# Performance work log

Measured on AMD Instinct MI355X. Metric: run time of the kernel, lower is better.

## Reference

```python
import jax, jax.numpy as jnp
import numpy as np

NEG = 1e9  # mask value added to already-selected positions (original uses -1e9)


def setup_inputs() -> dict:
    key = jax.random.key(0)
    ks = jax.random.split(key, 12)
    B, N, M = 8, 2048, 256
    s = 0.05  # keep gates/softmax in a sane range
    return dict(
        node_embedding=jax.random.normal(ks[0], (B, N, M), dtype=jnp.float32),
        z_g=jax.random.normal(ks[1], (B, M), dtype=jnp.float32) * s,
        decoder_init=jax.random.normal(ks[2], (M,), dtype=jnp.float32) * s,
        hidden0=jax.random.normal(ks[3], (M,), dtype=jnp.float32) * s,
        w_ih=jax.random.normal(ks[4], (4 * M, M), dtype=jnp.float32) * s,
        w_hh=jax.random.normal(ks[5], (4 * M, M), dtype=jnp.float32) * s,
        b_ih=jax.random.normal(ks[6], (4 * M,), dtype=jnp.float32) * s,
        b_hh=jax.random.normal(ks[7], (4 * M,), dtype=jnp.float32) * s,
        Wq=jax.random.normal(ks[8], (M, M), dtype=jnp.float32) * s,
        bq=jax.random.normal(ks[9], (M,), dtype=jnp.float32) * s,
        Wk=jax.random.normal(ks[10], (M, M), dtype=jnp.float32) * s,
        bk=jax.random.normal(ks[11], (M,), dtype=jnp.float32) * s,
    )


def reference(node_embedding, z_g, decoder_init, hidden0,
              w_ih, w_hh, b_ih, b_hh, Wq, bq, Wk, bk):
    # Returns the per-step masked softmax attention distributions [B, N, N]
    # (row t = distribution over boxes at decode step t; argmax of each row
    #  is the predicted order, and selected indices are masked out).
    N = node_embedding.shape[1]
    # LSTM input is the constant decoder_init every step -> precompute its proj.
    x_proj = decoder_init @ w_ih.T + b_ih  # [4M]

    def decode_one(z_g_b, node_emb_b):
        keys = node_emb_b @ Wk.T + bk  # [N, M] (self.key(node_embedding))

        def step(carry, _):
            h, c, used = carry
            # torch LSTMCell: gates ordered (i, f, g, o)
            gates = x_proj + h @ w_hh.T + b_hh  # [4M]
            i_g, f_g, g_g, o_g = jnp.split(gates, 4)
            i_g = jax.nn.sigmoid(i_g)
            f_g = jax.nn.sigmoid(f_g)
            g_g = jnp.tanh(g_g)
            o_g = jax.nn.sigmoid(o_g)
            c = f_g * c + i_g * g_g
            h = o_g * jnp.tanh(c)
            q = h @ Wq.T + bq                    # [M]
            scores = keys @ q                    # [N]
            scores = jnp.where(used, scores - NEG, scores)  # mask selected
            probs = jax.nn.softmax(scores)       # [N]
            idx = jnp.argmax(probs)              # top-1 pointer selection
            used = used.at[idx].set(True)
            return (h, c, used), probs

        init = (hidden0, z_g_b, jnp.zeros((N,), dtype=bool))
        _, probs = jax.lax.scan(step, init, None, length=N)
        return probs  # [N, N]

    return jax.vmap(decode_one)(z_g, node_embedding)  # [B, N, N]
```

## Files before the change

### kernel.cpp

```cpp
#include <hip/hip_runtime.h>
#include <cstdint>
#include <cstddef>

#define NB 8
#define NN 2048
#define MM 256

typedef unsigned long long u64;

__device__ __forceinline__ unsigned mapf(float f) {
  unsigned u = __float_as_uint(f + 0.f);
  return ((int)u >= 0) ? (u ^ 0x80000000u) : ~u;
}
__device__ __forceinline__ u64 shflx_u64(u64 v, int m) {
  unsigned lo = (unsigned)__shfl_xor((int)(unsigned)v, m);
  unsigned hi = (unsigned)__shfl_xor((int)(v >> 32), m);
  return ((u64)hi << 32) | lo;
}
__device__ __forceinline__ u64 agent_load(const u64* p) {
  return __hip_atomic_load(p, __ATOMIC_RELAXED, __HIP_MEMORY_SCOPE_AGENT);
}

__global__ __launch_bounds__(1024) void lstm_kernel(
    const float* __restrict__ z_g, const float* __restrict__ dec,
    const float* __restrict__ h0, const float* __restrict__ w_ih,
    const float* __restrict__ w_hh, const float* __restrict__ b_ih,
    const float* __restrict__ b_hh, float* __restrict__ Hall,
    u64* __restrict__ Pbuf)
{
  const int b = blockIdx.x;
  const int q = blockIdx.y;
  const int tid = threadIdx.x;
  const int w = tid >> 6;
  const int lane = tid & 63;
  const int rr = lane >> 3;
  const int c8 = lane & 7;
  const int lr = 8 * w + rr;
  const int g = lr >> 5;
  const int m = lr & 31;
  const int grow = g * 256 + 32 * q + m;

  __shared__ __align__(16) float hbuf[256];
  __shared__ __align__(16) float act[128];

  float wreg[32];
  {
    const float* wr = w_hh + (size_t)grow * MM + 32 * c8;
    #pragma unroll
    for (int jj = 0; jj < 8; ++jj) {
      float4 v = *(const float4*)(wr + 4 * ((jj + c8) & 7));
      wreg[4 * jj + 0] = v.x; wreg[4 * jj + 1] = v.y;
      wreg[4 * jj + 2] = v.z; wreg[4 * jj + 3] = v.w;
    }
  }

  float xb;
  {
    const float* wr = w_ih + (size_t)grow * MM + 32 * c8;
    float p = 0.f;
    #pragma unroll
    for (int i = 0; i < 8; ++i) {
      float4 wv = *(const float4*)(wr + 4 * i);
      float4 dv = *(const float4*)(dec + 32 * c8 + 4 * i);
      p += wv.x * dv.x + wv.y * dv.y + wv.z * dv.z + wv.w * dv.w;
    }
    p += __shfl_xor(p, 1); p += __shfl_xor(p, 2); p += __shfl_xor(p, 4);
    xb = p + b_ih[grow] + b_hh[grow];
  }

  float c_my = 0.f;
  if (tid < 32) c_my = z_g[b * MM + 32 * q + tid];
  if (tid < 256) hbuf[tid] = h0[tid];

  u64* Pb = Pbuf + (size_t)b * 512;
  float* Hb = Hall + (size_t)b * NN * MM + 32 * q;

  const bool own0 = ((lane >> 5) + 0) == q;
  const bool own1 = ((lane >> 5) + 2) == q;
  const bool own2 = ((lane >> 5) + 4) == q;
  const bool own3 = ((lane >> 5) + 6) == q;

  for (int tt = 0; tt < NN; ++tt) {
    if (tt > 0 && w == 0) {
      const u64* pa = Pb + ((tt & 1) << 8);
      const unsigned tg = (unsigned)tt;
      u64 a0, a1, a2, a3;
      for (;;) {
        a0 = agent_load(pa + lane);
        a1 = agent_load(pa + 64 + lane);
        a2 = agent_load(pa + 128 + lane);
        a3 = agent_load(pa + 192 + lane);
        const bool ok = (own0 | ((unsigned)(a0 >> 32) == tg))
                      & (own1 | ((unsigned)(a1 >> 32) == tg))
                      & (own2 | ((unsigned)(a2 >> 32) == tg))
                      & (own3 | ((unsigned)(a3 >> 32) == tg));
        if (__all((int)ok)) break;
      }
      if (!own0) hbuf[lane]       = __uint_as_float((unsigned)a0);
      if (!own1) hbuf[64 + lane]  = __uint_as_float((unsigned)a1);
      if (!own2) hbuf[128 + lane] = __uint_as_float((unsigned)a2);
      if (!own3) hbuf[192 + lane] = __uint_as_float((unsigned)a3);
    }
    __syncthreads();

    const float4* h4 = (const float4*)hbuf;
    float a0 = 0.f, a1 = 0.f, a2 = 0.f, a3 = 0.f;
    #pragma unroll
    for (int jj = 0; jj < 8; ++jj) {
      float4 hv = h4[8 * c8 + ((jj + c8) & 7)];
      a0 = fmaf(hv.x, wreg[4 * jj + 0], a0);
      a1 = fmaf(hv.y, wreg[4 * jj + 1], a1);
      a2 = fmaf(hv.z, wreg[4 * jj + 2], a2);
      a3 = fmaf(hv.w, wreg[4 * jj + 3], a3);
    }
    float s = (a0 + a1) + (a2 + a3);
    s += __shfl_xor(s, 1); s += __shfl_xor(s, 2); s += __shfl_xor(s, 4);
    const float gsum = s + xb;

    float a;
    if ((w >> 2) == 2) { const float e = __expf(-2.f * gsum); a = 2.f / (1.f + e) - 1.f; }
    else               { a = 1.f / (1.f + __expf(-gsum)); }
    if (c8 == 0) act[lr] = a;
    __syncthreads();

    if (tid < 32) {
      const float i_g = act[tid], f_g = act[32 + tid];
      const float g_g = act[64 + tid], o_g = act[96 + tid];
      c_my = f_g * c_my + i_g * g_g;
      const float e2 = __expf(-2.f * c_my);
      const float hn = o_g * (2.f / (1.f + e2) - 1.f);
      const u64 pk = ((u64)(unsigned)(tt + 1) << 32) | (u64)__float_as_uint(hn);
      __hip_atomic_store(Pb + (((tt + 1) & 1) << 8) + 32 * q + tid, pk,
                         __ATOMIC_RELAXED, __HIP_MEMORY_SCOPE_AGENT);
      hbuf[32 * q + tid] = hn;
      Hb[(size_t)tt * MM + tid] = hn;
    }
  }
}

__global__ __launch_bounds__(256) void gemm128(
    const float* __restrict__ A, const float* __restrict__ B,
    float* __restrict__ C, const float* __restrict__ bias,
    int K, int Ncol, long sA, long sB, long sC)
{
  __shared__ __align__(16) float As[32][132];
  __shared__ __align__(16) float Bs[32][132];
  const int tid = threadIdx.x;
  const int tx = tid & 15;
  const int ty = tid >> 4;
  const int row0 = blockIdx.y * 128;
  const int col0 = blockIdx.x * 128;
  const float* Ab = A + (size_t)blockIdx.z * (size_t)sA;
  const float* Bb = B + (size_t)blockIdx.z * (size_t)sB;
  float* Cb = C + (size_t)blockIdx.z * (size_t)sC;

  float acc[8][8];
  #pragma unroll
  for (int i = 0; i < 8; ++i)
    #pragma unroll
    for (int jj = 0; jj < 8; ++jj) acc[i][jj] = 0.f;

  for (int k0 = 0; k0 < K; k0 += 32) {
    #pragma unroll
    for (int it = 0; it < 4; ++it) {
      const int idx = tid + it * 256;
      const int r = idx >> 3;
      const int c4 = (idx & 7) << 2;
      float4 va = *(const float4*)(Ab + (size_t)(row0 + r) * K + k0 + c4);
      float4 vb = *(const float4*)(Bb + (size_t)(col0 + r) * K + k0 + c4);
      As[c4 + 0][r] = va.x; As[c4 + 1][r] = va.y;
      As[c4 + 2][r] = va.z; As[c4 + 3][r] = va.w;
      Bs[c4 + 0][r] = vb.x; Bs[c4 + 1][r] = vb.y;
      Bs[c4 + 2][r] = vb.z; Bs[c4 + 3][r] = vb.w;
    }
    __syncthreads();
    #pragma unroll
    for (int kk = 0; kk < 32; ++kk) {
      float4 a0 = *(const float4*)&As[kk][ty * 4];
      float4 a1 = *(const float4*)&As[kk][64 + ty * 4];
      float4 b0 = *(const float4*)&Bs[kk][tx * 4];
      float4 b1 = *(const float4*)&Bs[kk][64 + tx * 4];
      const float av[8] = {a0.x, a0.y, a0.z, a0.w, a1.x, a1.y, a1.z, a1.w};
      const float bv[8] = {b0.x, b0.y, b0.z, b0.w, b1.x, b1.y, b1.z, b1.w};
      #pragma unroll
      for (int i = 0; i < 8; ++i)
        #pragma unroll
        for (int jj = 0; jj < 8; ++jj)
          acc[i][jj] = fmaf(av[i], bv[jj], acc[i][jj]);
    }
    __syncthreads();
  }

  #pragma unroll
  for (int i = 0; i < 8; ++i) {
    const int r = row0 + ((i < 4) ? (ty * 4 + i) : (64 + ty * 4 + i - 4));
    float* cp = Cb + (size_t)r * Ncol + col0;
    float4 o0, o1;
    float* o0p = &o0.x; float* o1p = &o1.x;
    #pragma unroll
    for (int jj = 0; jj < 4; ++jj) {
      float v0 = acc[i][jj], v1 = acc[i][jj + 4];
      if (bias) {
        v0 += bias[col0 + tx * 4 + jj];
        v1 += bias[col0 + 64 + tx * 4 + jj];
      }
      o0p[jj] = v0; o1p[jj] = v1;
    }
    *(float4*)(cp + tx * 4) = o0;
    *(float4*)(cp + 64 + tx * 4) = o1;
  }
}

__global__ __launch_bounds__(512) void select_block(
    const float* __restrict__ S, int* __restrict__ sel)
{
  const int b = blockIdx.x;
  const int tid = threadIdx.x;
  const int w = tid >> 6;
  const int lane = tid & 63;
  const float* Sb = S + (size_t)b * NN * NN + 4 * tid;
  int* selb = sel + b * NN;

  __shared__ u64 partial[2][8];

  for (int i = tid; i < NN; i += 512) selb[i] = 0x7fffffff;
  __syncthreads();

  unsigned mybits = 0;
  const unsigned base = 2047u - 4u * (unsigned)tid;

  auto stepf = [&](float4 v, int t) {
    u64 k0 = (mybits & 1u) ? 0 : (((u64)mapf(v.x) << 32) | (base - 0u));
    u64 k1 = (mybits & 2u) ? 0 : (((u64)mapf(v.y) << 32) | (base - 1u));
    u64 k2 = (mybits & 4u) ? 0 : (((u64)mapf(v.z) << 32) | (base - 2u));
    u64 k3 = (mybits & 8u) ? 0 : (((u64)mapf(v.w) << 32) | (base - 3u));
    u64 k = k0 > k1 ? k0 : k1;
    if (k2 > k) k = k2;
    if (k3 > k) k = k3;
    #pragma unroll
    for (int off = 1; off < 64; off <<= 1) {
      u64 o = shflx_u64(k, off);
      if (o > k) k = o;
    }
    if (lane == 0) partial[t & 1][w] = k;
    __syncthreads();
    u64 pk = partial[t & 1][lane & 7];
    #pragma unroll
    for (int off = 1; off < 8; off <<= 1) {
      u64 o = shflx_u64(pk, off);
      if (o > pk) pk = o;
    }
    const int idx = 2047 - (int)(pk & 0x7ff);
    if ((idx >> 2) == tid) mybits |= 1u << (idx & 3);
    if (tid == 0) selb[idx] = t;
  };

  float4 r0 = *(const float4*)(Sb + (size_t)0 * NN);
  float4 r1 = *(const float4*)(Sb + (size_t)1 * NN);
  float4 r2 = *(const float4*)(Sb + (size_t)2 * NN);
  float4 r3 = *(const float4*)(Sb + (size_t)3 * NN);
  for (int t = 0; t < NN; t += 4) {
    const size_t p4 = (size_t)((t + 4 < NN) ? t + 4 : NN - 1) * NN;
    const size_t p5 = (size_t)((t + 5 < NN) ? t + 5 : NN - 1) * NN;
    const size_t p6 = (size_t)((t + 6 < NN) ? t + 6 : NN - 1) * NN;
    const size_t p7 = (size_t)((t + 7 < NN) ? t + 7 : NN - 1) * NN;
    stepf(r0, t);     r0 = *(const float4*)(Sb + p4);
    stepf(r1, t + 1); r1 = *(const float4*)(Sb + p5);
    stepf(r2, t + 2); r2 = *(const float4*)(Sb + p6);
    stepf(r3, t + 3); r3 = *(const float4*)(Sb + p7);
  }
}

__global__ __launch_bounds__(256) void softmax_kernel(
    float* __restrict__ out, const int* __restrict__ sel)
{
  const int t = blockIdx.x;
  const int b = blockIdx.y;
  const int tid = threadIdx.x;
  float* row = out + ((size_t)b * NN + t) * NN;
  const int* selb = sel + b * NN;
  __shared__ float red[8];

  float v[8];
  int sl[8];
  #pragma unroll
  for (int u = 0; u < 2; ++u) {
    float4 f = *(const float4*)(row + u * 1024 + tid * 4);
    int4 s4 = *(const int4*)(selb + u * 1024 + tid * 4);
    v[u * 4 + 0] = f.x; v[u * 4 + 1] = f.y; v[u * 4 + 2] = f.z; v[u * 4 + 3] = f.w;
    sl[u * 4 + 0] = s4.x; sl[u * 4 + 1] = s4.y; sl[u * 4 + 2] = s4.z; sl[u * 4 + 3] = s4.w;
  }

  float mx = -3.0e38f;
  #pragma unroll
  for (int e = 0; e < 8; ++e)
    if (sl[e] >= t) mx = fmaxf(mx, v[e]);
  #pragma unroll
  for (int off = 1; off < 64; off <<= 1) mx = fmaxf(mx, __shfl_xor(mx, off));
  if ((tid & 63) == 0) red[tid >> 6] = mx;
  __syncthreads();
  mx = fmaxf(fmaxf(red[0], red[1]), fmaxf(red[2], red[3]));

  float e8[8];
  float sum = 0.f;
  #pragma unroll
  for (int e = 0; e < 8; ++e) {
    float ex = (sl[e] >= t) ? __expf(v[e] - mx) : 0.f;
    e8[e] = ex;
    sum += ex;
  }
  #pragma unroll
  for (int off = 1; off < 64; off <<= 1) sum += __shfl_xor(sum, off);
  if ((tid & 63) == 0) red[4 + (tid >> 6)] = sum;
  __syncthreads();
  sum = red[4] + red[5] + red[6] + red[7];
  const float inv = 1.f / sum;

  #pragma unroll
  for (int u = 0; u < 2; ++u) {
    float4 o;
    o.x = e8[u * 4 + 0] * inv; o.y = e8[u * 4 + 1] * inv;
    o.z = e8[u * 4 + 2] * inv; o.w = e8[u * 4 + 3] * inv;
    *(float4*)(row + u * 1024 + tid * 4) = o;
  }
}

extern "C" void kernel_launch(void* const* d_in, const int* in_sizes, int n_in,
                              void* d_out, int out_size, void* d_ws, size_t ws_size,
                              hipStream_t stream)
{
  (void)in_sizes; (void)n_in; (void)out_size; (void)ws_size;
  const float* emb  = (const float*)d_in[0];
  const float* z_g  = (const float*)d_in[1];
  const float* dec  = (const float*)d_in[2];
  const float* h0   = (const float*)d_in[3];
  const float* w_ih = (const float*)d_in[4];
  const float* w_hh = (const float*)d_in[5];
  const float* b_ih = (const float*)d_in[6];
  const float* b_hh = (const float*)d_in[7];
  const float* Wq   = (const float*)d_in[8];
  const float* bq   = (const float*)d_in[9];
  const float* Wk   = (const float*)d_in[10];
  const float* bk   = (const float*)d_in[11];
  float* out = (float*)d_out;
  float* ws  = (float*)d_ws;

  float* keys  = ws;
  float* Q     = ws + 4194304;
  u64*   Pbuf  = (u64*)(ws + 8388608);
  int*   sel   = (int*)(ws + 8396800);
  float* Hall  = out;

  hipMemsetAsync(Pbuf, 0, 4096 * sizeof(u64), stream);

  lstm_kernel<<<dim3(NB, 8), 1024, 0, stream>>>(
      z_g, dec, h0, w_ih, w_hh, b_ih, b_hh, Hall, Pbuf);

  gemm128<<<dim3(MM / 128, (NB * NN) / 128, 1), 256, 0, stream>>>(
      Hall, Wq, Q, bq, MM, MM, 0, 0, 0);

  gemm128<<<dim3(MM / 128, (NB * NN) / 128, 1), 256, 0, stream>>>(
      emb, Wk, keys, bk, MM, MM, 0, 0, 0);

  gemm128<<<dim3(NN / 128, NN / 128, NB), 256, 0, stream>>>(
      Q, keys, out, nullptr, MM, NN,
      (long)NN * MM, (long)NN * MM, (long)NN * NN);

  select_block<<<NB, 512, 0, stream>>>(out, sel);

  softmax_kernel<<<dim3(NN, NB), 256, 0, stream>>>(out, sel);
}
```

Before: 4.707 ms.

## Interleave two batch LSTM chains per block to hide cross-block sync latency

Each LSTM workgroup now processes two independent batch samples in alternation, so the global-memory handshake for one sample's hidden state is issued and polled while the other sample's matvec runs. This halves the grid to 32 blocks and double-buffers hbuf and cell state per chain. It aims to hide the inter-block spin-wait latency that dominates the serial recurrence, at the cost of twice as many serial steps per block.

```diff
diff --git a/kernel.cpp b/kernel.cpp
--- a/kernel.cpp
+++ b/kernel.cpp
@@ -28,7 +28,7 @@
     const float* __restrict__ b_hh, float* __restrict__ Hall,
     u64* __restrict__ Pbuf)
 {
-  const int b = blockIdx.x;
+  const int p = blockIdx.x;
   const int q = blockIdx.y;
   const int tid = threadIdx.x;
   const int w = tid >> 6;
@@ -40,7 +40,7 @@
   const int m = lr & 31;
   const int grow = g * 256 + 32 * q + m;
 
-  __shared__ __align__(16) float hbuf[256];
+  __shared__ __align__(16) float hbuf[2][256];
   __shared__ __align__(16) float act[128];
 
   float wreg[32];
@@ -57,23 +57,28 @@
   float xb;
   {
     const float* wr = w_ih + (size_t)grow * MM + 32 * c8;
-    float p = 0.f;
+    float pc = 0.f;
     #pragma unroll
     for (int i = 0; i < 8; ++i) {
       float4 wv = *(const float4*)(wr + 4 * i);
       float4 dv = *(const float4*)(dec + 32 * c8 + 4 * i);
-      p += wv.x * dv.x + wv.y * dv.y + wv.z * dv.z + wv.w * dv.w;
-    }
-    p += __shfl_xor(p, 1); p += __shfl_xor(p, 2); p += __shfl_xor(p, 4);
-    xb = p + b_ih[grow] + b_hh[grow];
-  }
-
-  float c_my = 0.f;
-  if (tid < 32) c_my = z_g[b * MM + 32 * q + tid];
-  if (tid < 256) hbuf[tid] = h0[tid];
-
-  u64* Pb = Pbuf + (size_t)b * 512;
-  float* Hb = Hall + (size_t)b * NN * MM + 32 * q;
+      pc += wv.x * dv.x + wv.y * dv.y + wv.z * dv.z + wv.w * dv.w;
+    }
+    pc += __shfl_xor(pc, 1); pc += __shfl_xor(pc, 2); pc += __shfl_xor(pc, 4);
+    xb = pc + b_ih[grow] + b_hh[grow];
+  }
+
+  float cmy[2] = {0.f, 0.f};
+  if (tid < 32) {
+    cmy[0] = z_g[(2 * p + 0) * MM + 32 * q + tid];
+    cmy[1] = z_g[(2 * p + 1) * MM + 32 * q + tid];
+  }
+  if (tid < 256) { hbuf[0][tid] = h0[tid]; hbuf[1][tid] = h0[tid]; }
+
+  u64* Pb0 = Pbuf + (size_t)(2 * p + 0) * 512;
+  u64* Pb1 = Pbuf + (size_t)(2 * p + 1) * 512;
+  float* Hb0 = Hall + (size_t)(2 * p + 0) * NN * MM + 32 * q;
+  float* Hb1 = Hall + (size_t)(2 * p + 1) * NN * MM + 32 * q;
 
   const bool own0 = ((lane >> 5) + 0) == q;
   const bool own1 = ((lane >> 5) + 2) == q;
@@ -81,59 +86,79 @@
   const bool own3 = ((lane >> 5) + 6) == q;
 
   for (int tt = 0; tt < NN; ++tt) {
-    if (tt > 0 && w == 0) {
-      const u64* pa = Pb + ((tt & 1) << 8);
-      const unsigned tg = (unsigned)tt;
-      u64 a0, a1, a2, a3;
-      for (;;) {
+    #pragma unroll
+    for (int ch = 0; ch < 2; ++ch) {
+      const int och = 1 - ch;
+      const int ot = tt + ch;
+      const bool otv = (ot >= 1) && (ot < NN);
+      u64* Pbo = (ch == 0) ? Pb1 : Pb0;
+
+      __syncthreads();
+
+      u64 a0 = 0, a1 = 0, a2 = 0, a3 = 0;
+      const u64* pa = Pbo + ((ot & 1) << 8);
+      if (w == 1 && otv) {
         a0 = agent_load(pa + lane);
         a1 = agent_load(pa + 64 + lane);
         a2 = agent_load(pa + 128 + lane);
         a3 = agent_load(pa + 192 + lane);
-        const bool ok = (own0 | ((unsigned)(a0 >> 32) == tg))
-                      & (own1 | ((unsigned)(a1 >> 32) == tg))
-                      & (own2 | ((unsigned)(a2 >> 32) == tg))
-                      & (own3 | ((unsigned)(a3 >> 32) == tg));
-        if (__all((int)ok)) break;
-      }
-      if (!own0) hbuf[lane]       = __uint_as_float((unsigned)a0);
-      if (!own1) hbuf[64 + lane]  = __uint_as_float((unsigned)a1);
-      if (!own2) hbuf[128 + lane] = __uint_as_float((unsigned)a2);
-      if (!own3) hbuf[192 + lane] = __uint_as_float((unsigned)a3);
-    }
-    __syncthreads();
-
-    const float4* h4 = (const float4*)hbuf;
-    float a0 = 0.f, a1 = 0.f, a2 = 0.f, a3 = 0.f;
-    #pragma unroll
-    for (int jj = 0; jj < 8; ++jj) {
-      float4 hv = h4[8 * c8 + ((jj + c8) & 7)];
-      a0 = fmaf(hv.x, wreg[4 * jj + 0], a0);
-      a1 = fmaf(hv.y, wreg[4 * jj + 1], a1);
-      a2 = fmaf(hv.z, wreg[4 * jj + 2], a2);
-      a3 = fmaf(hv.w, wreg[4 * jj + 3], a3);
-    }
-    float s = (a0 + a1) + (a2 + a3);
-    s += __shfl_xor(s, 1); s += __shfl_xor(s, 2); s += __shfl_xor(s, 4);
-    const float gsum = s + xb;
-
-    float a;
-    if ((w >> 2) == 2) { const float e = __expf(-2.f * gsum); a = 2.f / (1.f + e) - 1.f; }
-    else               { a = 1.f / (1.f + __expf(-gsum)); }
-    if (c8 == 0) act[lr] = a;
-    __syncthreads();
-
-    if (tid < 32) {
-      const float i_g = act[tid], f_g = act[32 + tid];
-      const float g_g = act[64 + tid], o_g = act[96 + tid];
-      c_my = f_g * c_my + i_g * g_g;
-      const float e2 = __expf(-2.f * c_my);
-      const float hn = o_g * (2.f / (1.f + e2) - 1.f);
-      const u64 pk = ((u64)(unsigned)(tt + 1) << 32) | (u64)__float_as_uint(hn);
-      __hip_atomic_store(Pb + (((tt + 1) & 1) << 8) + 32 * q + tid, pk,
-                         __ATOMIC_RELAXED, __HIP_MEMORY_SCOPE_AGENT);
-      hbuf[32 * q + tid] = hn;
-      Hb[(size_t)tt * MM + tid] = hn;
+      }
+
+      const float4* h4 = (const float4*)hbuf[ch];
+      float s0 = 0.f, s1 = 0.f, s2 = 0.f, s3 = 0.f;
+      #pragma unroll
+      for (int jj = 0; jj < 8; ++jj) {
+        float4 hv = h4[8 * c8 + ((jj + c8) & 7)];
+        s0 = fmaf(hv.x, wreg[4 * jj + 0], s0);
+        s1 = fmaf(hv.y, wreg[4 * jj + 1], s1);
+        s2 = fmaf(hv.z, wreg[4 * jj + 2], s2);
+        s3 = fmaf(hv.w, wreg[4 * jj + 3], s3);
+      }
+      float s = (s0 + s1) + (s2 + s3);
+      s += __shfl_xor(s, 1); s += __shfl_xor(s, 2); s += __shfl_xor(s, 4);
+      const float gsum = s + xb;
+
+      float a;
+      if ((w >> 2) == 2) { const float e = __expf(-2.f * gsum); a = 2.f / (1.f + e) - 1.f; }
+      else               { a = 1.f / (1.f + __expf(-gsum)); }
+      if (c8 == 0) act[lr] = a;
+      __syncthreads();
+
+      if (tid < 32) {
+        const float i_g = act[tid], f_g = act[32 + tid];
+        const float g_g = act[64 + tid], o_g = act[96 + tid];
+        float c = cmy[ch];
+        c = f_g * c + i_g * g_g;
+        cmy[ch] = c;
+        const float e2 = __expf(-2.f * c);
+        const float hn = o_g * (2.f / (1.f + e2) - 1.f);
+        const u64 pk = ((u64)(unsigned)(tt + 1) << 32) | (u64)__float_as_uint(hn);
+        u64* Pbc = (ch == 0) ? Pb0 : Pb1;
+        float* Hbc = (ch == 0) ? Hb0 : Hb1;
+        __hip_atomic_store(Pbc + (((tt + 1) & 1) << 8) + 32 * q + tid, pk,
+                           __ATOMIC_RELAXED, __HIP_MEMORY_SCOPE_AGENT);
+        hbuf[ch][32 * q + tid] = hn;
+        Hbc[(size_t)tt * MM + tid] = hn;
+      }
+
+      if (w == 1 && otv) {
+        const unsigned tg = (unsigned)ot;
+        for (;;) {
+          const bool ok = (own0 | ((unsigned)(a0 >> 32) == tg))
+                        & (own1 | ((unsigned)(a1 >> 32) == tg))
+                        & (own2 | ((unsigned)(a2 >> 32) == tg))
+                        & (own3 | ((unsigned)(a3 >> 32) == tg));
+          if (__all((int)ok)) break;
+          a0 = agent_load(pa + lane);
+          a1 = agent_load(pa + 64 + lane);
+          a2 = agent_load(pa + 128 + lane);
+          a3 = agent_load(pa + 192 + lane);
+        }
+        if (!own0) hbuf[och][lane]       = __uint_as_float((unsigned)a0);
+        if (!own1) hbuf[och][64 + lane]  = __uint_as_float((unsigned)a1);
+        if (!own2) hbuf[och][128 + lane] = __uint_as_float((unsigned)a2);
+        if (!own3) hbuf[och][192 + lane] = __uint_as_float((unsigned)a3);
+      }
     }
   }
 }
@@ -353,7 +378,7 @@
 
   hipMemsetAsync(Pbuf, 0, 4096 * sizeof(u64), stream);
 
-  lstm_kernel<<<dim3(NB, 8), 1024, 0, stream>>>(
+  lstm_kernel<<<dim3(4, 8), 1024, 0, stream>>>(
       z_g, dec, h0, w_ih, w_hh, b_ih, b_hh, Hall, Pbuf);
 
   gemm128<<<dim3(MM / 128, (NB * NN) / 128, 1), 256, 0, stream>>>(
```

Measured after the change: 6.046 ms. 28.5% more time.

## Select two decode steps per barrier via top-2 reduction; move LSTM cell update to wave 1

Applied to the files above, without the earlier changes.

The selection kernel now processes two consecutive argmax steps per block barrier. For the second row it reduces the top two keys, so the step-B winner can exclude the index just chosen in step A. This halves the number of __syncthreads and cross-wave reductions in a serial chain, at the cost of three shuffled 64-bit values per reduction level. Separately, the LSTM cell update moves from wave 0 to wave 1 so it no longer shares a wave with the polling loop.

```diff
diff --git a/kernel.cpp b/kernel.cpp
--- a/kernel.cpp
+++ b/kernel.cpp
@@ -69,7 +69,7 @@
   }
 
   float c_my = 0.f;
-  if (tid < 32) c_my = z_g[b * MM + 32 * q + tid];
+  if (w == 1 && lane < 32) c_my = z_g[b * MM + 32 * q + lane];
   if (tid < 256) hbuf[tid] = h0[tid];
 
   u64* Pb = Pbuf + (size_t)b * 512;
@@ -123,17 +123,17 @@
     if (c8 == 0) act[lr] = a;
     __syncthreads();
 
-    if (tid < 32) {
-      const float i_g = act[tid], f_g = act[32 + tid];
-      const float g_g = act[64 + tid], o_g = act[96 + tid];
+    if (w == 1 && lane < 32) {
+      const float i_g = act[lane], f_g = act[32 + lane];
+      const float g_g = act[64 + lane], o_g = act[96 + lane];
       c_my = f_g * c_my + i_g * g_g;
       const float e2 = __expf(-2.f * c_my);
       const float hn = o_g * (2.f / (1.f + e2) - 1.f);
       const u64 pk = ((u64)(unsigned)(tt + 1) << 32) | (u64)__float_as_uint(hn);
-      __hip_atomic_store(Pb + (((tt + 1) & 1) << 8) + 32 * q + tid, pk,
+      __hip_atomic_store(Pb + (((tt + 1) & 1) << 8) + 32 * q + lane, pk,
                          __ATOMIC_RELAXED, __HIP_MEMORY_SCOPE_AGENT);
-      hbuf[32 * q + tid] = hn;
-      Hb[(size_t)tt * MM + tid] = hn;
+      hbuf[32 * q + lane] = hn;
+      Hb[(size_t)tt * MM + lane] = hn;
     }
   }
 }
@@ -221,7 +221,7 @@
   const float* Sb = S + (size_t)b * NN * NN + 4 * tid;
   int* selb = sel + b * NN;
 
-  __shared__ u64 partial[2][8];
+  __shared__ u64 pA[2][8], pB1[2][8], pB2[2][8];
 
   for (int i = tid; i < NN; i += 512) selb[i] = 0x7fffffff;
   __syncthreads();
@@ -229,30 +229,61 @@
   unsigned mybits = 0;
   const unsigned base = 2047u - 4u * (unsigned)tid;
 
-  auto stepf = [&](float4 v, int t) {
-    u64 k0 = (mybits & 1u) ? 0 : (((u64)mapf(v.x) << 32) | (base - 0u));
-    u64 k1 = (mybits & 2u) ? 0 : (((u64)mapf(v.y) << 32) | (base - 1u));
-    u64 k2 = (mybits & 4u) ? 0 : (((u64)mapf(v.z) << 32) | (base - 2u));
-    u64 k3 = (mybits & 8u) ? 0 : (((u64)mapf(v.w) << 32) | (base - 3u));
-    u64 k = k0 > k1 ? k0 : k1;
-    if (k2 > k) k = k2;
-    if (k3 > k) k = k3;
+  auto keys4 = [&](float4 v, u64* k) {
+    k[0] = (mybits & 1u) ? 0 : (((u64)mapf(v.x) << 32) | (base - 0u));
+    k[1] = (mybits & 2u) ? 0 : (((u64)mapf(v.y) << 32) | (base - 1u));
+    k[2] = (mybits & 4u) ? 0 : (((u64)mapf(v.z) << 32) | (base - 2u));
+    k[3] = (mybits & 8u) ? 0 : (((u64)mapf(v.w) << 32) | (base - 3u));
+  };
+
+  auto pairf = [&](float4 vA, float4 vB, int t) {
+    const int buf = (t >> 1) & 1;
+    u64 ka[4], kb[4];
+    keys4(vA, ka);
+    keys4(vB, kb);
+
+    u64 A = ka[0] > ka[1] ? ka[0] : ka[1];
+    if (ka[2] > A) A = ka[2];
+    if (ka[3] > A) A = ka[3];
+
+    u64 m01 = kb[0] > kb[1] ? kb[0] : kb[1];
+    u64 n01 = kb[0] > kb[1] ? kb[1] : kb[0];
+    u64 m23 = kb[2] > kb[3] ? kb[2] : kb[3];
+    u64 n23 = kb[2] > kb[3] ? kb[3] : kb[2];
+    u64 B1, B2;
+    if (m01 > m23) { B1 = m01; B2 = (m23 > n01) ? m23 : n01; }
+    else           { B1 = m23; B2 = (m01 > n23) ? m01 : n23; }
+
     #pragma unroll
     for (int off = 1; off < 64; off <<= 1) {
-      u64 o = shflx_u64(k, off);
-      if (o > k) k = o;
-    }
-    if (lane == 0) partial[t & 1][w] = k;
+      u64 oA = shflx_u64(A, off);
+      u64 o1 = shflx_u64(B1, off);
+      u64 o2 = shflx_u64(B2, off);
+      if (oA > A) A = oA;
+      if (o1 > B1) { B2 = (B1 > o2) ? B1 : o2; B1 = o1; }
+      else if (o1 > B2) { B2 = o1; }
+    }
+    if (lane == 0) { pA[buf][w] = A; pB1[buf][w] = B1; pB2[buf][w] = B2; }
     __syncthreads();
-    u64 pk = partial[t & 1][lane & 7];
+    u64 FA = pA[buf][lane & 7];
+    u64 C1 = pB1[buf][lane & 7];
+    u64 C2 = pB2[buf][lane & 7];
     #pragma unroll
     for (int off = 1; off < 8; off <<= 1) {
-      u64 o = shflx_u64(pk, off);
-      if (o > pk) pk = o;
-    }
-    const int idx = 2047 - (int)(pk & 0x7ff);
-    if ((idx >> 2) == tid) mybits |= 1u << (idx & 3);
-    if (tid == 0) selb[idx] = t;
+      u64 oA = shflx_u64(FA, off);
+      u64 o1 = shflx_u64(C1, off);
+      u64 o2 = shflx_u64(C2, off);
+      if (oA > FA) FA = oA;
+      if (o1 > C1) { C2 = (C1 > o2) ? C1 : o2; C1 = o1; }
+      else if (o1 > C2) { C2 = o1; }
+    }
+
+    const int selA = 2047 - (int)(FA & 0x7ffu);
+    const u64 chosen = ((C1 & 0x7ffu) != (FA & 0x7ffu)) ? C1 : C2;
+    const int selB = 2047 - (int)(chosen & 0x7ffu);
+    if ((selA >> 2) == tid) mybits |= 1u << (selA & 3);
+    if ((selB >> 2) == tid) mybits |= 1u << (selB & 3);
+    if (tid == 0) { selb[selA] = t; selb[selB] = t + 1; }
   };
 
   float4 r0 = *(const float4*)(Sb + (size_t)0 * NN);
@@ -264,10 +295,10 @@
     const size_t p5 = (size_t)((t + 5 < NN) ? t + 5 : NN - 1) * NN;
     const size_t p6 = (size_t)((t + 6 < NN) ? t + 6 : NN - 1) * NN;
     const size_t p7 = (size_t)((t + 7 < NN) ? t + 7 : NN - 1) * NN;
-    stepf(r0, t);     r0 = *(const float4*)(Sb + p4);
-    stepf(r1, t + 1); r1 = *(const float4*)(Sb + p5);
-    stepf(r2, t + 2); r2 = *(const float4*)(Sb + p6);
-    stepf(r3, t + 3); r3 = *(const float4*)(Sb + p7);
+    pairf(r0, r1, t);     r0 = *(const float4*)(Sb + p4);
+    r1 = *(const float4*)(Sb + p5);
+    pairf(r2, r3, t + 2); r2 = *(const float4*)(Sb + p6);
+    r3 = *(const float4*)(Sb + p7);
   }
 }
 
```

New measurement: 5.283 ms. +12.3%, slower.
